# Performance work log

Hardware: AMD Instinct MI355X
Metric: run time of the kernel (lower is better)

The kernel has to match this reference:

```python
import jax, jax.numpy as jnp
import numpy as np

NUM_EXPERTS = 8
EXPERTS_PER_TOK = 2

def setup_inputs() -> dict:
    key = jax.random.key(0)
    k1, k2, k3, k4, k5 = jax.random.split(key, 5)
    B, T, D, F, E = 4, 1024, 2048, 1024, NUM_EXPERTS
    return {
        "x": jax.random.normal(k1, (B, T, D), dtype=jnp.float32),
        "router_w": jax.random.normal(k2, (D, E), dtype=jnp.float32) * 0.02,
        "gate_proj": jax.random.normal(k3, (E, D, F), dtype=jnp.float32) * 0.02,
        "up_proj": jax.random.normal(k4, (E, D, F), dtype=jnp.float32) * 0.02,
        "down_proj": jax.random.normal(k5, (E, F, D), dtype=jnp.float32) * 0.02,
    }

def reference(x, router_w, gate_proj, up_proj, down_proj):
    E, K = NUM_EXPERTS, EXPERTS_PER_TOK
    # Router: softmax over experts, take top-k, renormalize.
    scores = jnp.einsum('btd,de->bte', x, router_w).astype(jnp.float32)
    routing_weights, routing_idx = jax.lax.top_k(jax.nn.softmax(scores, axis=-1), K)
    routing_weights = (routing_weights / jnp.sum(routing_weights, axis=-1, keepdims=True)).astype(x.dtype)
    # one_hot: [B,T,K,E]. Sum over K gives 0/1 dispatch mask [B,T,E]
    # (top-k indices are distinct). Weighted sum gives combine weights.
    onehot = jax.nn.one_hot(routing_idx, E, dtype=x.dtype)
    dispatch_mask = jnp.sum(onehot, axis=2)                      # [B,T,E]
    combine_weights = jnp.einsum('btke,btk->bte', onehot, routing_weights)
    # Dense masked dispatch (same math as original einsum with size-1 I axis).
    dispatched = x[:, :, None, :] * dispatch_mask[..., None]     # [B,T,E,D]
    # SwiGLU FFN for every expert, batched over E.
    gate = jnp.einsum('bted,edf->btef', dispatched, gate_proj)
    up = jnp.einsum('bted,edf->btef', dispatched, up_proj)
    act = jax.nn.silu(gate) * up                                 # [B,T,E,F]
    expert_out = jnp.einsum('btef,efd->bted', act, down_proj)    # [B,T,E,D]
    # Combine: weights already include the dispatch mask via one-hot.
    return jnp.einsum('bted,bte->btd', expert_out, combine_weights)
```

## Files before the change

### kernel.cpp

```cpp
#include <hip/hip_runtime.h>
#include <stdint.h>

#define BT 4096
#define DMODEL 2048
#define FDIM 1024
#define NEXP 8
#define NA (BT * 2)
#define MAXTILES 72
#define NB1 (FDIM / 128)
#define NB2 (DMODEL / 128)
#define GRID1 (MAXTILES * NB1)
#define GRID2 (MAXTILES * NB2)

typedef __attribute__((ext_vector_type(8))) __bf16 bf16x8;
typedef __attribute__((ext_vector_type(4))) float f32x4;

__device__ __forceinline__ unsigned short f2bf(float f) {
  union { float f; unsigned int u; } v; v.f = f;
  unsigned int u = v.u;
  unsigned int r = (u + 0x7fffu + ((u >> 16) & 1u)) >> 16;
  return (unsigned short)r;
}
__device__ __forceinline__ float bf2f(unsigned short h) {
  union { unsigned int u; float f; } v; v.u = ((unsigned int)h) << 16;
  return v.f;
}

__device__ __forceinline__ void g2l16(const void* g, void* l) {
  __builtin_amdgcn_global_load_lds((const __attribute__((address_space(1))) void*)g,
                                   (__attribute__((address_space(3))) void*)l, 16, 0, 0);
}


__global__ void k_router(const float* __restrict__ x, const float* __restrict__ rw,
                         unsigned short* __restrict__ xbf,
                         int* __restrict__ tok_e, float* __restrict__ tok_w) {
  int wid = threadIdx.x >> 6;
  int lane = threadIdx.x & 63;
  int t = blockIdx.x * 4 + wid;
  float acc[8];
#pragma unroll
  for (int e = 0; e < 8; e++) acc[e] = 0.0f;
  const float* xr = x + (size_t)t * DMODEL;
  unsigned short* xbr = xbf + (size_t)t * DMODEL;
#pragma unroll
  for (int d0 = lane * 4; d0 < DMODEL; d0 += 256) {
    float4 xv = *(const float4*)(xr + d0);
    ushort4 o = make_ushort4(f2bf(xv.x), f2bf(xv.y), f2bf(xv.z), f2bf(xv.w));
    *(ushort4*)(xbr + d0) = o;
    const float* xs = &xv.x;
#pragma unroll
    for (int j = 0; j < 4; j++) {
      const float4* r4 = (const float4*)(rw + (size_t)(d0 + j) * NEXP);
      float4 ra = r4[0], rb = r4[1];
      float xj = xs[j];
      acc[0] += xj * ra.x; acc[1] += xj * ra.y; acc[2] += xj * ra.z; acc[3] += xj * ra.w;
      acc[4] += xj * rb.x; acc[5] += xj * rb.y; acc[6] += xj * rb.z; acc[7] += xj * rb.w;
    }
  }
#pragma unroll
  for (int e = 0; e < 8; e++) {
    float v = acc[e];
#pragma unroll
    for (int off = 32; off > 0; off >>= 1) v += __shfl_xor(v, off);
    acc[e] = v;
  }
  if (lane == 0) {
    int e0 = 0; float s0 = acc[0];
#pragma unroll
    for (int e = 1; e < 8; e++) if (acc[e] > s0) { s0 = acc[e]; e0 = e; }
    int e1 = (e0 == 0) ? 1 : 0; float s1 = acc[e1];
#pragma unroll
    for (int e = 0; e < 8; e++) if (e != e0 && acc[e] > s1) { s1 = acc[e]; e1 = e; }
    float w0 = 1.0f / (1.0f + __expf(s1 - s0));
    tok_e[t * 2] = e0; tok_e[t * 2 + 1] = e1;
    tok_w[t * 2] = w0; tok_w[t * 2 + 1] = 1.0f - w0;
  }
}

__global__ void k_scanbuild(const int* __restrict__ tok_e, int* __restrict__ offsets,
                            int* __restrict__ tile_e, int* __restrict__ tile_y,
                            int* __restrict__ ntiles, int* __restrict__ cursors) {
  __shared__ int hist[NEXP];
  int tid = threadIdx.x;
  if (tid < NEXP) hist[tid] = 0;
  __syncthreads();
  for (int i = tid; i < NA; i += 256) atomicAdd(&hist[tok_e[i]], 1);
  __syncthreads();
  if (tid == 0) {
    int s = 0;
    for (int e = 0; e < NEXP; e++) { offsets[e] = s; s += hist[e]; }
    offsets[NEXP] = s;
    int idx = 0;
    for (int e = 0; e < NEXP; e++) {
      int nt = (hist[e] + 127) >> 7;
      for (int y = 0; y < nt; y++) { tile_e[idx] = e; tile_y[idx] = y; idx++; }
    }
    *ntiles = idx;
    for (int i = idx; i < MAXTILES; i++) { tile_e[i] = 0; tile_y[i] = 0; }
  }
  if (tid < NEXP) cursors[tid] = 0;
}

__global__ void k_scatter(const int* __restrict__ tok_e, const float* __restrict__ tok_w,
                          const int* __restrict__ offsets, int* __restrict__ cursors,
                          int* __restrict__ assign_token, float* __restrict__ assign_w,
                          int* __restrict__ tok2pos) {
  int i = blockIdx.x * 256 + threadIdx.x;
  if (i >= NA) return;
  int e = tok_e[i];
  int pos = offsets[e] + atomicAdd(&cursors[e], 1);
  assign_token[pos] = i >> 1;
  assign_w[pos] = tok_w[i];
  tok2pos[i] = pos;
}

__global__ void k_transpose_all(const float* __restrict__ gw, const float* __restrict__ uw,
                                const float* __restrict__ dw,
                                unsigned short* __restrict__ wtg, unsigned short* __restrict__ wtu,
                                unsigned short* __restrict__ wtd) {
  __shared__ float tile[64][65];
  int z = blockIdx.y;
  const float* src; unsigned short* dst; int N;
  if (z < 8)       { src = gw + (size_t)z * DMODEL * FDIM;        dst = wtg + (size_t)z * DMODEL * FDIM;        N = FDIM; }
  else if (z < 16) { src = uw + (size_t)(z - 8) * DMODEL * FDIM;  dst = wtu + (size_t)(z - 8) * DMODEL * FDIM;  N = FDIM; }
  else             { src = dw + (size_t)(z - 16) * FDIM * DMODEL; dst = wtd + (size_t)(z - 16) * FDIM * DMODEL; N = DMODEL; }
  int ntx = N >> 6;
  int bx = blockIdx.x;
  int n0 = (bx % ntx) * 64, k0 = (bx / ntx) * 64;
  int rr = threadIdx.x >> 4, cc = threadIdx.x & 15;
#pragma unroll
  for (int i = 0; i < 4; i++) {
    int k = rr + i * 16;
    float4 v = *(const float4*)(src + (size_t)(k0 + k) * N + n0 + cc * 4);
    tile[k][cc * 4 + 0] = v.x; tile[k][cc * 4 + 1] = v.y;
    tile[k][cc * 4 + 2] = v.z; tile[k][cc * 4 + 3] = v.w;
  }
  __syncthreads();
  int K = (z < 16) ? DMODEL : FDIM;
#pragma unroll
  for (int i = 0; i < 4; i++) {
    int n = rr + i * 16;
    ushort4 o = make_ushort4(f2bf(tile[cc * 4 + 0][n]), f2bf(tile[cc * 4 + 1][n]),
                             f2bf(tile[cc * 4 + 2][n]), f2bf(tile[cc * 4 + 3][n]));
    *(ushort4*)(dst + (size_t)(n0 + n) * K + k0 + cc * 4) = o;
  }
}


__global__ __launch_bounds__(256, 2) void k_gemm1(
    const unsigned short* __restrict__ xbf,
    const unsigned short* __restrict__ wtg,
    const unsigned short* __restrict__ wtu,
    const int* __restrict__ offsets,
    const int* __restrict__ tile_e, const int* __restrict__ tile_y,
    const int* __restrict__ ntiles,
    const int* __restrict__ assign_token,
    unsigned short* __restrict__ act) {
  const int flat = blockIdx.x;
  const int wgid = (flat & 7) * (GRID1 / 8) + (flat >> 3);
  const int ti = wgid % MAXTILES;
  const int nb = wgid / MAXTILES;
  if (ti >= *ntiles) return;
  const int e = tile_e[ti];
  const int row_beg = offsets[e], row_end = offsets[e + 1];
  const int m_base = row_beg + tile_y[ti] * 128;
  const int n_base = nb * 128;

  __shared__ unsigned short As[128][64];
  __shared__ unsigned short Bg[128][64];
  __shared__ unsigned short Bu[128][64];

  const int tid = threadIdx.x;
  const int lane = tid & 63, wid = tid >> 6;
  const int wr = wid >> 1, wc = wid & 1;
  const int srow = wid * 8 + (lane >> 3);
  const int scol_d = (lane & 7) * 8;
  const int scol_s = ((lane & 7) ^ (lane >> 3)) * 8;
  const int sw = (lane & 7) * 8;

  const unsigned short* wg_e = wtg + (size_t)e * FDIM * DMODEL;
  const unsigned short* wu_e = wtu + (size_t)e * FDIM * DMODEL;

  size_t arow[4];
#pragma unroll
  for (int i = 0; i < 4; i++) {
    int slot = m_base + i * 32 + srow;
    if (slot >= row_end) slot = row_end - 1;
    arow[i] = (size_t)assign_token[slot] * DMODEL;
  }

  f32x4 accg[4][4], accu[4][4];
#pragma unroll
  for (int m = 0; m < 4; m++)
#pragma unroll
    for (int n = 0; n < 4; n++) {
      accg[m][n] = f32x4{0.f, 0.f, 0.f, 0.f};
      accu[m][n] = f32x4{0.f, 0.f, 0.f, 0.f};
    }

  for (int k0 = 0; k0 < DMODEL; k0 += 64) {
    __syncthreads();
#pragma unroll
    for (int i = 0; i < 4; i++)
      g2l16(xbf + arow[i] + k0 + scol_s, &As[i * 32 + srow][scol_d]);
#pragma unroll
    for (int i = 0; i < 4; i++)
      g2l16(wg_e + (size_t)(n_base + i * 32 + srow) * DMODEL + k0 + scol_s, &Bg[i * 32 + srow][scol_d]);
#pragma unroll
    for (int i = 0; i < 4; i++)
      g2l16(wu_e + (size_t)(n_base + i * 32 + srow) * DMODEL + k0 + scol_s, &Bu[i * 32 + srow][scol_d]);
    __syncthreads();

#pragma unroll
    for (int kk = 0; kk < 2; kk++) {
      const int ko = kk * 32 + (lane >> 4) * 8;
      bf16x8 a[4], bg[4], bu[4];
#pragma unroll
      for (int m = 0; m < 4; m++)
        a[m] = *(const bf16x8*)&As[wr * 64 + m * 16 + (lane & 15)][ko ^ sw];
#pragma unroll
      for (int n = 0; n < 4; n++) {
        bg[n] = *(const bf16x8*)&Bg[wc * 64 + n * 16 + (lane & 15)][ko ^ sw];
        bu[n] = *(const bf16x8*)&Bu[wc * 64 + n * 16 + (lane & 15)][ko ^ sw];
      }
#pragma unroll
      for (int m = 0; m < 4; m++)
#pragma unroll
        for (int n = 0; n < 4; n++) {
          accg[m][n] = __builtin_amdgcn_mfma_f32_16x16x32_bf16(a[m], bg[n], accg[m][n], 0, 0, 0);
          accu[m][n] = __builtin_amdgcn_mfma_f32_16x16x32_bf16(a[m], bu[n], accu[m][n], 0, 0, 0);
        }
    }
  }

  const int cr = (lane >> 4) * 4;
  const int ccc = lane & 15;
#pragma unroll
  for (int m = 0; m < 4; m++) {
#pragma unroll
    for (int j = 0; j < 4; j++) {
      int slot = m_base + wr * 64 + m * 16 + cr + j;
      if (slot < row_end) {
        unsigned short* dst = act + (size_t)slot * FDIM + n_base + wc * 64 + ccc;
#pragma unroll
        for (int n = 0; n < 4; n++) {
          float g = accg[m][n][j], u = accu[m][n][j];
          float h = (g / (1.0f + __expf(-g))) * u;
          dst[n * 16] = f2bf(h);
        }
      }
    }
  }
}


__global__ __launch_bounds__(256, 2) void k_gemm2(
    const unsigned short* __restrict__ act,
    const unsigned short* __restrict__ wtd,
    const int* __restrict__ offsets,
    const int* __restrict__ tile_e, const int* __restrict__ tile_y,
    const int* __restrict__ ntiles,
    const float* __restrict__ assign_w,
    unsigned short* __restrict__ out_pa) {
  const int flat = blockIdx.x;
  const int wgid = (flat & 7) * (GRID2 / 8) + (flat >> 3);
  const int ti = wgid % MAXTILES;
  const int nb = wgid / MAXTILES;
  if (ti >= *ntiles) return;
  const int e = tile_e[ti];
  const int row_beg = offsets[e], row_end = offsets[e + 1];
  const int m_base = row_beg + tile_y[ti] * 128;
  const int n_base = nb * 128;

  __shared__ unsigned short As[128][64];
  __shared__ unsigned short Bs[128][64];

  const int tid = threadIdx.x;
  const int lane = tid & 63, wid = tid >> 6;
  const int wr = wid >> 1, wc = wid & 1;
  const int srow = wid * 8 + (lane >> 3);
  const int scol_d = (lane & 7) * 8;
  const int scol_s = ((lane & 7) ^ (lane >> 3)) * 8;
  const int sw = (lane & 7) * 8;

  const unsigned short* wd_e = wtd + (size_t)e * DMODEL * FDIM;

  size_t arow[4];
#pragma unroll
  for (int i = 0; i < 4; i++) {
    int slot = m_base + i * 32 + srow;
    if (slot >= row_end) slot = row_end - 1;
    arow[i] = (size_t)slot * FDIM;
  }

  f32x4 acc[4][4];
#pragma unroll
  for (int m = 0; m < 4; m++)
#pragma unroll
    for (int n = 0; n < 4; n++) acc[m][n] = f32x4{0.f, 0.f, 0.f, 0.f};

  for (int k0 = 0; k0 < FDIM; k0 += 64) {
    __syncthreads();
#pragma unroll
    for (int i = 0; i < 4; i++)
      g2l16(act + arow[i] + k0 + scol_s, &As[i * 32 + srow][scol_d]);
#pragma unroll
    for (int i = 0; i < 4; i++)
      g2l16(wd_e + (size_t)(n_base + i * 32 + srow) * FDIM + k0 + scol_s, &Bs[i * 32 + srow][scol_d]);
    __syncthreads();

#pragma unroll
    for (int kk = 0; kk < 2; kk++) {
      const int ko = kk * 32 + (lane >> 4) * 8;
      bf16x8 a[4], b[4];
#pragma unroll
      for (int m = 0; m < 4; m++)
        a[m] = *(const bf16x8*)&As[wr * 64 + m * 16 + (lane & 15)][ko ^ sw];
#pragma unroll
      for (int n = 0; n < 4; n++)
        b[n] = *(const bf16x8*)&Bs[wc * 64 + n * 16 + (lane & 15)][ko ^ sw];
#pragma unroll
      for (int m = 0; m < 4; m++)
#pragma unroll
        for (int n = 0; n < 4; n++)
          acc[m][n] = __builtin_amdgcn_mfma_f32_16x16x32_bf16(a[m], b[n], acc[m][n], 0, 0, 0);
    }
  }

  const int cr = (lane >> 4) * 4;
  const int ccc = lane & 15;
#pragma unroll
  for (int m = 0; m < 4; m++) {
#pragma unroll
    for (int j = 0; j < 4; j++) {
      int slot = m_base + wr * 64 + m * 16 + cr + j;
      if (slot < row_end) {
        float w = assign_w[slot];
        unsigned short* dst = out_pa + (size_t)slot * DMODEL + n_base + wc * 64 + ccc;
#pragma unroll
        for (int n = 0; n < 4; n++)
          dst[n * 16] = f2bf(acc[m][n][j] * w);
      }
    }
  }
}

__global__ void k_combine(const unsigned short* __restrict__ out_pa,
                          const int* __restrict__ tok2pos,
                          float* __restrict__ out) {
  int t = blockIdx.x;
  int p0 = tok2pos[t * 2], p1 = tok2pos[t * 2 + 1];
  int c = threadIdx.x;
  const ushort4* a = (const ushort4*)(out_pa + (size_t)p0 * DMODEL + c * 8);
  const ushort4* b = (const ushort4*)(out_pa + (size_t)p1 * DMODEL + c * 8);
  ushort4 a0 = a[0], a1 = a[1], b0 = b[0], b1 = b[1];
  float* o = out + (size_t)t * DMODEL + c * 8;
  o[0] = bf2f(a0.x) + bf2f(b0.x);
  o[1] = bf2f(a0.y) + bf2f(b0.y);
  o[2] = bf2f(a0.z) + bf2f(b0.z);
  o[3] = bf2f(a0.w) + bf2f(b0.w);
  o[4] = bf2f(a1.x) + bf2f(b1.x);
  o[5] = bf2f(a1.y) + bf2f(b1.y);
  o[6] = bf2f(a1.z) + bf2f(b1.z);
  o[7] = bf2f(a1.w) + bf2f(b1.w);
}


extern "C" void kernel_launch(void* const* d_in, const int* in_sizes, int n_in,
                              void* d_out, int out_size, void* d_ws, size_t ws_size,
                              hipStream_t stream) {
  const float* x  = (const float*)d_in[0];
  const float* rw = (const float*)d_in[1];
  const float* gw = (const float*)d_in[2];
  const float* uw = (const float*)d_in[3];
  const float* dw = (const float*)d_in[4];
  float* out = (float*)d_out;

  char* ws = (char*)d_ws;
  size_t off = 0;
  auto alloc = [&](size_t bytes) {
    size_t o = off;
    off += (bytes + 255) & ~(size_t)255;
    return o;
  };
  unsigned short* xbf    = (unsigned short*)(ws + alloc((size_t)BT * DMODEL * 2));
  unsigned short* wtg    = (unsigned short*)(ws + alloc((size_t)NEXP * FDIM * DMODEL * 2));
  unsigned short* wtu    = (unsigned short*)(ws + alloc((size_t)NEXP * FDIM * DMODEL * 2));
  unsigned short* wtd    = (unsigned short*)(ws + alloc((size_t)NEXP * DMODEL * FDIM * 2));
  unsigned short* act    = (unsigned short*)(ws + alloc((size_t)NA * FDIM * 2));
  unsigned short* out_pa = (unsigned short*)(ws + alloc((size_t)NA * DMODEL * 2));
  int*   offsets = (int*)(ws + alloc((NEXP + 1) * 4));
  int*   cursors = (int*)(ws + alloc(NEXP * 4));
  int*   tok_e   = (int*)(ws + alloc(NA * 4));
  float* tok_w   = (float*)(ws + alloc(NA * 4));
  int*   assign_token = (int*)(ws + alloc(NA * 4));
  float* assign_w     = (float*)(ws + alloc(NA * 4));
  int*   tok2pos      = (int*)(ws + alloc(NA * 4));
  int*   tile_e       = (int*)(ws + alloc(MAXTILES * 4));
  int*   tile_y       = (int*)(ws + alloc(MAXTILES * 4));
  int*   ntiles       = (int*)(ws + alloc(4));
  if (off > ws_size) return;

  k_router<<<BT / 4, 256, 0, stream>>>(x, rw, xbf, tok_e, tok_w);
  k_scanbuild<<<1, 256, 0, stream>>>(tok_e, offsets, tile_e, tile_y, ntiles, cursors);
  k_scatter<<<NA / 256, 256, 0, stream>>>(tok_e, tok_w, offsets, cursors,
                                          assign_token, assign_w, tok2pos);
  k_transpose_all<<<dim3(512, 24), 256, 0, stream>>>(gw, uw, dw, wtg, wtu, wtd);
  k_gemm1<<<GRID1, 256, 0, stream>>>(xbf, wtg, wtu, offsets,
                                     tile_e, tile_y, ntiles, assign_token, act);
  k_gemm2<<<GRID2, 256, 0, stream>>>(act, wtd, offsets,
                                     tile_e, tile_y, ntiles, assign_w, out_pa);
  k_combine<<<BT, 256, 0, stream>>>(out_pa, tok2pos, out);
}
```

Baseline: 320.5 us.

## Double-buffer grouped GEMMs with 256-row tiles and 512-thread blocks

New measurement: 344.9 us. 7.6% more time.

```diff
diff --git a/kernel.cpp b/kernel.cpp
--- a/kernel.cpp
+++ b/kernel.cpp
@@ -6,14 +6,20 @@
 #define FDIM 1024
 #define NEXP 8
 #define NA (BT * 2)
-#define MAXTILES 72
+#define MAXT 40
 #define NB1 (FDIM / 128)
-#define NB2 (DMODEL / 128)
-#define GRID1 (MAXTILES * NB1)
-#define GRID2 (MAXTILES * NB2)
+#define NB2 (DMODEL / 256)
+#define GRID1 (MAXT * NB1)
+#define GRID2 (MAXT * NB2)
+#define NT1 (DMODEL / 64)
+#define NT2 (FDIM / 64)
 
 typedef __attribute__((ext_vector_type(8))) __bf16 bf16x8;
 typedef __attribute__((ext_vector_type(4))) float f32x4;
+
+#define FENCE() asm volatile("" ::: "memory")
+#define BARRIER() do { FENCE(); __builtin_amdgcn_s_barrier(); FENCE(); } while (0)
+#define WAITVM0() asm volatile("s_waitcnt vmcnt(0)" ::: "memory")
 
 __device__ __forceinline__ unsigned short f2bf(float f) {
   union { float f; unsigned int u; } v; v.f = f;
@@ -93,11 +99,11 @@
     offsets[NEXP] = s;
     int idx = 0;
     for (int e = 0; e < NEXP; e++) {
-      int nt = (hist[e] + 127) >> 7;
+      int nt = (hist[e] + 255) >> 8;
       for (int y = 0; y < nt; y++) { tile_e[idx] = e; tile_y[idx] = y; idx++; }
     }
     *ntiles = idx;
-    for (int i = idx; i < MAXTILES; i++) { tile_e[i] = 0; tile_y[i] = 0; }
+    for (int i = idx; i < MAXT; i++) { tile_e[i] = 0; tile_y[i] = 0; }
   }
   if (tid < NEXP) cursors[tid] = 0;
 }
@@ -148,7 +154,7 @@
 }
 
 
-__global__ __launch_bounds__(256, 2) void k_gemm1(
+__global__ __launch_bounds__(512, 2) void k_gemm1(
     const unsigned short* __restrict__ xbf,
     const unsigned short* __restrict__ wtg,
     const unsigned short* __restrict__ wtu,
@@ -159,92 +165,114 @@
     unsigned short* __restrict__ act) {
   const int flat = blockIdx.x;
   const int wgid = (flat & 7) * (GRID1 / 8) + (flat >> 3);
-  const int ti = wgid % MAXTILES;
-  const int nb = wgid / MAXTILES;
+  const int ti = wgid % MAXT;
+  const int nb = wgid / MAXT;
   if (ti >= *ntiles) return;
   const int e = tile_e[ti];
   const int row_beg = offsets[e], row_end = offsets[e + 1];
-  const int m_base = row_beg + tile_y[ti] * 128;
+  const int m_base = row_beg + tile_y[ti] * 256;
   const int n_base = nb * 128;
 
-  __shared__ unsigned short As[128][64];
-  __shared__ unsigned short Bg[128][64];
-  __shared__ unsigned short Bu[128][64];
+  __shared__ unsigned short As[2][256][64];
+  __shared__ unsigned short Bg[2][128][64];
+  __shared__ unsigned short Bu[2][128][64];
 
   const int tid = threadIdx.x;
   const int lane = tid & 63, wid = tid >> 6;
-  const int wr = wid >> 1, wc = wid & 1;
-  const int srow = wid * 8 + (lane >> 3);
-  const int scol_d = (lane & 7) * 8;
-  const int scol_s = ((lane & 7) ^ (lane >> 3)) * 8;
+  const int wm = wid >> 2, wn = wid & 3;
+  const int l15 = lane & 15;
+  const int srow = tid >> 3;
+  const int scol_d = (tid & 7) * 8;
+  const int scol_s = ((tid & 7) ^ (srow & 7)) * 8;
   const int sw = (lane & 7) * 8;
 
-  const unsigned short* wg_e = wtg + (size_t)e * FDIM * DMODEL;
-  const unsigned short* wu_e = wtu + (size_t)e * FDIM * DMODEL;
+  const unsigned short* wg_e = wtg + (size_t)e * FDIM * DMODEL + (size_t)n_base * DMODEL;
+  const unsigned short* wu_e = wtu + (size_t)e * FDIM * DMODEL + (size_t)n_base * DMODEL;
 
   size_t arow[4];
 #pragma unroll
   for (int i = 0; i < 4; i++) {
-    int slot = m_base + i * 32 + srow;
+    int slot = m_base + i * 64 + srow;
     if (slot >= row_end) slot = row_end - 1;
     arow[i] = (size_t)assign_token[slot] * DMODEL;
   }
 
-  f32x4 accg[4][4], accu[4][4];
-#pragma unroll
-  for (int m = 0; m < 4; m++)
-#pragma unroll
-    for (int n = 0; n < 4; n++) {
+  f32x4 accg[8][2], accu[8][2];
+#pragma unroll
+  for (int m = 0; m < 8; m++)
+#pragma unroll
+    for (int n = 0; n < 2; n++) {
       accg[m][n] = f32x4{0.f, 0.f, 0.f, 0.f};
       accu[m][n] = f32x4{0.f, 0.f, 0.f, 0.f};
     }
 
-  for (int k0 = 0; k0 < DMODEL; k0 += 64) {
-    __syncthreads();
+  auto stageA = [&](int buf, int k0) {
 #pragma unroll
     for (int i = 0; i < 4; i++)
-      g2l16(xbf + arow[i] + k0 + scol_s, &As[i * 32 + srow][scol_d]);
-#pragma unroll
-    for (int i = 0; i < 4; i++)
-      g2l16(wg_e + (size_t)(n_base + i * 32 + srow) * DMODEL + k0 + scol_s, &Bg[i * 32 + srow][scol_d]);
-#pragma unroll
-    for (int i = 0; i < 4; i++)
-      g2l16(wu_e + (size_t)(n_base + i * 32 + srow) * DMODEL + k0 + scol_s, &Bu[i * 32 + srow][scol_d]);
-    __syncthreads();
+      g2l16(xbf + arow[i] + k0 + scol_s, &As[buf][i * 64 + srow][scol_d]);
+  };
+  auto stageB = [&](int buf, int k0) {
+#pragma unroll
+    for (int i = 0; i < 2; i++)
+      g2l16(wg_e + (size_t)(i * 64 + srow) * DMODEL + k0 + scol_s, &Bg[buf][i * 64 + srow][scol_d]);
+#pragma unroll
+    for (int i = 0; i < 2; i++)
+      g2l16(wu_e + (size_t)(i * 64 + srow) * DMODEL + k0 + scol_s, &Bu[buf][i * 64 + srow][scol_d]);
+  };
+
+  stageA(0, 0); stageB(0, 0);
+  WAITVM0(); BARRIER();
+
+  for (int t = 0; t < NT1; ++t) {
+    const int cur = t & 1, nxt = cur ^ 1;
+    const int k1 = (t + 1) * 64;
+    const bool pref = (t + 1 < NT1);
 
 #pragma unroll
     for (int kk = 0; kk < 2; kk++) {
       const int ko = kk * 32 + (lane >> 4) * 8;
-      bf16x8 a[4], bg[4], bu[4];
-#pragma unroll
-      for (int m = 0; m < 4; m++)
-        a[m] = *(const bf16x8*)&As[wr * 64 + m * 16 + (lane & 15)][ko ^ sw];
-#pragma unroll
-      for (int n = 0; n < 4; n++) {
-        bg[n] = *(const bf16x8*)&Bg[wc * 64 + n * 16 + (lane & 15)][ko ^ sw];
-        bu[n] = *(const bf16x8*)&Bu[wc * 64 + n * 16 + (lane & 15)][ko ^ sw];
-      }
-#pragma unroll
-      for (int m = 0; m < 4; m++)
-#pragma unroll
-        for (int n = 0; n < 4; n++) {
-          accg[m][n] = __builtin_amdgcn_mfma_f32_16x16x32_bf16(a[m], bg[n], accg[m][n], 0, 0, 0);
-          accu[m][n] = __builtin_amdgcn_mfma_f32_16x16x32_bf16(a[m], bu[n], accu[m][n], 0, 0, 0);
-        }
+      bf16x8 a[8];
+#pragma unroll
+      for (int m = 0; m < 8; m++)
+        a[m] = *(const bf16x8*)&As[cur][wm * 128 + m * 16 + l15][ko ^ sw];
+      bf16x8 b0 = *(const bf16x8*)&Bg[cur][wn * 32 + l15][ko ^ sw];
+      bf16x8 b1 = *(const bf16x8*)&Bg[cur][wn * 32 + 16 + l15][ko ^ sw];
+      if (pref && kk == 0) stageA(nxt, k1);
+      BARRIER();
+      __builtin_amdgcn_s_setprio(1);
+#pragma unroll
+      for (int m = 0; m < 8; m++) {
+        accg[m][0] = __builtin_amdgcn_mfma_f32_16x16x32_bf16(a[m], b0, accg[m][0], 0, 0, 0);
+        accg[m][1] = __builtin_amdgcn_mfma_f32_16x16x32_bf16(a[m], b1, accg[m][1], 0, 0, 0);
+      }
+      __builtin_amdgcn_s_setprio(0);
+      BARRIER();
+      b0 = *(const bf16x8*)&Bu[cur][wn * 32 + l15][ko ^ sw];
+      b1 = *(const bf16x8*)&Bu[cur][wn * 32 + 16 + l15][ko ^ sw];
+      if (pref && kk == 0) stageB(nxt, k1);
+      BARRIER();
+      __builtin_amdgcn_s_setprio(1);
+#pragma unroll
+      for (int m = 0; m < 8; m++) {
+        accu[m][0] = __builtin_amdgcn_mfma_f32_16x16x32_bf16(a[m], b0, accu[m][0], 0, 0, 0);
+        accu[m][1] = __builtin_amdgcn_mfma_f32_16x16x32_bf16(a[m], b1, accu[m][1], 0, 0, 0);
+      }
+      __builtin_amdgcn_s_setprio(0);
+      if (kk == 1 && pref) WAITVM0();
+      BARRIER();
     }
   }
 
   const int cr = (lane >> 4) * 4;
-  const int ccc = lane & 15;
-#pragma unroll
-  for (int m = 0; m < 4; m++) {
+#pragma unroll
+  for (int m = 0; m < 8; m++) {
 #pragma unroll
     for (int j = 0; j < 4; j++) {
-      int slot = m_base + wr * 64 + m * 16 + cr + j;
+      int slot = m_base + wm * 128 + m * 16 + cr + j;
       if (slot < row_end) {
-        unsigned short* dst = act + (size_t)slot * FDIM + n_base + wc * 64 + ccc;
-#pragma unroll
-        for (int n = 0; n < 4; n++) {
+        unsigned short* dst = act + (size_t)slot * FDIM + n_base + wn * 32 + l15;
+#pragma unroll
+        for (int n = 0; n < 2; n++) {
           float g = accg[m][n][j], u = accu[m][n][j];
           float h = (g / (1.0f + __expf(-g))) * u;
           dst[n * 16] = f2bf(h);
@@ -255,7 +283,7 @@
 }
 
 
-__global__ __launch_bounds__(256, 2) void k_gemm2(
+__global__ __launch_bounds__(512, 2) void k_gemm2(
     const unsigned short* __restrict__ act,
     const unsigned short* __restrict__ wtd,
     const int* __restrict__ offsets,
@@ -265,79 +293,105 @@
     unsigned short* __restrict__ out_pa) {
   const int flat = blockIdx.x;
   const int wgid = (flat & 7) * (GRID2 / 8) + (flat >> 3);
-  const int ti = wgid % MAXTILES;
-  const int nb = wgid / MAXTILES;
+  const int ti = wgid % MAXT;
+  const int nb = wgid / MAXT;
   if (ti >= *ntiles) return;
   const int e = tile_e[ti];
   const int row_beg = offsets[e], row_end = offsets[e + 1];
-  const int m_base = row_beg + tile_y[ti] * 128;
-  const int n_base = nb * 128;
-
-  __shared__ unsigned short As[128][64];
-  __shared__ unsigned short Bs[128][64];
+  const int m_base = row_beg + tile_y[ti] * 256;
+  const int n_base = nb * 256;
+
+  __shared__ unsigned short As[2][256][64];
+  __shared__ unsigned short Bs[2][256][64];
 
   const int tid = threadIdx.x;
   const int lane = tid & 63, wid = tid >> 6;
-  const int wr = wid >> 1, wc = wid & 1;
-  const int srow = wid * 8 + (lane >> 3);
-  const int scol_d = (lane & 7) * 8;
-  const int scol_s = ((lane & 7) ^ (lane >> 3)) * 8;
+  const int wm = wid >> 2, wn = wid & 3;
+  const int l15 = lane & 15;
+  const int srow = tid >> 3;
+  const int scol_d = (tid & 7) * 8;
+  const int scol_s = ((tid & 7) ^ (srow & 7)) * 8;
   const int sw = (lane & 7) * 8;
 
-  const unsigned short* wd_e = wtd + (size_t)e * DMODEL * FDIM;
+  const unsigned short* wd_e = wtd + (size_t)e * DMODEL * FDIM + (size_t)n_base * FDIM;
 
   size_t arow[4];
 #pragma unroll
   for (int i = 0; i < 4; i++) {
-    int slot = m_base + i * 32 + srow;
+    int slot = m_base + i * 64 + srow;
     if (slot >= row_end) slot = row_end - 1;
     arow[i] = (size_t)slot * FDIM;
   }
 
-  f32x4 acc[4][4];
-#pragma unroll
-  for (int m = 0; m < 4; m++)
+  f32x4 acc[8][4];
+#pragma unroll
+  for (int m = 0; m < 8; m++)
 #pragma unroll
     for (int n = 0; n < 4; n++) acc[m][n] = f32x4{0.f, 0.f, 0.f, 0.f};
 
-  for (int k0 = 0; k0 < FDIM; k0 += 64) {
-    __syncthreads();
+  auto stageA = [&](int buf, int k0) {
 #pragma unroll
     for (int i = 0; i < 4; i++)
-      g2l16(act + arow[i] + k0 + scol_s, &As[i * 32 + srow][scol_d]);
+      g2l16(act + arow[i] + k0 + scol_s, &As[buf][i * 64 + srow][scol_d]);
+  };
+  auto stageB = [&](int buf, int k0) {
 #pragma unroll
     for (int i = 0; i < 4; i++)
-      g2l16(wd_e + (size_t)(n_base + i * 32 + srow) * FDIM + k0 + scol_s, &Bs[i * 32 + srow][scol_d]);
-    __syncthreads();
+      g2l16(wd_e + (size_t)(i * 64 + srow) * FDIM + k0 + scol_s, &Bs[buf][i * 64 + srow][scol_d]);
+  };
+
+  stageA(0, 0); stageB(0, 0);
+  WAITVM0(); BARRIER();
+
+  for (int t = 0; t < NT2; ++t) {
+    const int cur = t & 1, nxt = cur ^ 1;
+    const int k1 = (t + 1) * 64;
+    const bool pref = (t + 1 < NT2);
 
 #pragma unroll
     for (int kk = 0; kk < 2; kk++) {
       const int ko = kk * 32 + (lane >> 4) * 8;
-      bf16x8 a[4], b[4];
-#pragma unroll
-      for (int m = 0; m < 4; m++)
-        a[m] = *(const bf16x8*)&As[wr * 64 + m * 16 + (lane & 15)][ko ^ sw];
-#pragma unroll
-      for (int n = 0; n < 4; n++)
-        b[n] = *(const bf16x8*)&Bs[wc * 64 + n * 16 + (lane & 15)][ko ^ sw];
-#pragma unroll
-      for (int m = 0; m < 4; m++)
-#pragma unroll
-        for (int n = 0; n < 4; n++)
-          acc[m][n] = __builtin_amdgcn_mfma_f32_16x16x32_bf16(a[m], b[n], acc[m][n], 0, 0, 0);
+      bf16x8 a[8];
+#pragma unroll
+      for (int m = 0; m < 8; m++)
+        a[m] = *(const bf16x8*)&As[cur][wm * 128 + m * 16 + l15][ko ^ sw];
+      bf16x8 b0 = *(const bf16x8*)&Bs[cur][wn * 64 + l15][ko ^ sw];
+      bf16x8 b1 = *(const bf16x8*)&Bs[cur][wn * 64 + 16 + l15][ko ^ sw];
+      if (pref && kk == 0) stageA(nxt, k1);
+      BARRIER();
+      __builtin_amdgcn_s_setprio(1);
+#pragma unroll
+      for (int m = 0; m < 8; m++) {
+        acc[m][0] = __builtin_amdgcn_mfma_f32_16x16x32_bf16(a[m], b0, acc[m][0], 0, 0, 0);
+        acc[m][1] = __builtin_amdgcn_mfma_f32_16x16x32_bf16(a[m], b1, acc[m][1], 0, 0, 0);
+      }
+      __builtin_amdgcn_s_setprio(0);
+      BARRIER();
+      b0 = *(const bf16x8*)&Bs[cur][wn * 64 + 32 + l15][ko ^ sw];
+      b1 = *(const bf16x8*)&Bs[cur][wn * 64 + 48 + l15][ko ^ sw];
+      if (pref && kk == 0) stageB(nxt, k1);
+      BARRIER();
+      __builtin_amdgcn_s_setprio(1);
+#pragma unroll
+      for (int m = 0; m < 8; m++) {
+        acc[m][2] = __builtin_amdgcn_mfma_f32_16x16x32_bf16(a[m], b0, acc[m][2], 0, 0, 0);
+        acc[m][3] = __builtin_amdgcn_mfma_f32_16x16x32_bf16(a[m], b1, acc[m][3], 0, 0, 0);
+      }
+      __builtin_amdgcn_s_setprio(0);
+      if (kk == 1 && pref) WAITVM0();
+      BARRIER();
     }
   }
 
   const int cr = (lane >> 4) * 4;
-  const int ccc = lane & 15;
-#pragma unroll
-  for (int m = 0; m < 4; m++) {
+#pragma unroll
+  for (int m = 0; m < 8; m++) {
 #pragma unroll
     for (int j = 0; j < 4; j++) {
-      int slot = m_base + wr * 64 + m * 16 + cr + j;
+      int slot = m_base + wm * 128 + m * 16 + cr + j;
       if (slot < row_end) {
         float w = assign_w[slot];
-        unsigned short* dst = out_pa + (size_t)slot * DMODEL + n_base + wc * 64 + ccc;
+        unsigned short* dst = out_pa + (size_t)slot * DMODEL + n_base + wn * 64 + l15;
 #pragma unroll
         for (int n = 0; n < 4; n++)
           dst[n * 16] = f2bf(acc[m][n][j] * w);
@@ -397,8 +451,8 @@
   int*   assign_token = (int*)(ws + alloc(NA * 4));
   float* assign_w     = (float*)(ws + alloc(NA * 4));
   int*   tok2pos      = (int*)(ws + alloc(NA * 4));
-  int*   tile_e       = (int*)(ws + alloc(MAXTILES * 4));
-  int*   tile_y       = (int*)(ws + alloc(MAXTILES * 4));
+  int*   tile_e       = (int*)(ws + alloc(MAXT * 4));
+  int*   tile_y       = (int*)(ws + alloc(MAXT * 4));
   int*   ntiles       = (int*)(ws + alloc(4));
   if (off > ws_size) return;
 
@@ -407,9 +461,9 @@
   k_scatter<<<NA / 256, 256, 0, stream>>>(tok_e, tok_w, offsets, cursors,
                                           assign_token, assign_w, tok2pos);
   k_transpose_all<<<dim3(512, 24), 256, 0, stream>>>(gw, uw, dw, wtg, wtu, wtd);
-  k_gemm1<<<GRID1, 256, 0, stream>>>(xbf, wtg, wtu, offsets,
+  k_gemm1<<<GRID1, 512, 0, stream>>>(xbf, wtg, wtu, offsets,
                                      tile_e, tile_y, ntiles, assign_token, act);
-  k_gemm2<<<GRID2, 256, 0, stream>>>(act, wtd, offsets,
+  k_gemm2<<<GRID2, 512, 0, stream>>>(act, wtd, offsets,
                                      tile_e, tile_y, ntiles, assign_w, out_pa);
   k_combine<<<BT, 256, 0, stream>>>(out_pa, tok2pos, out);
 }
```

## Interleave gate/up weights into one B matrix and raise GEMM occupancy

Applied to the files above, without the earlier changes.

Measured after the change: 301.0 us. 6.1% less time.

```diff
diff --git a/kernel.cpp b/kernel.cpp
--- a/kernel.cpp
+++ b/kernel.cpp
@@ -7,10 +7,6 @@
 #define NEXP 8
 #define NA (BT * 2)
 #define MAXTILES 72
-#define NB1 (FDIM / 128)
-#define NB2 (DMODEL / 128)
-#define GRID1 (MAXTILES * NB1)
-#define GRID2 (MAXTILES * NB2)
 
 typedef __attribute__((ext_vector_type(8))) __bf16 bf16x8;
 typedef __attribute__((ext_vector_type(4))) float f32x4;
@@ -117,14 +113,14 @@
 
 __global__ void k_transpose_all(const float* __restrict__ gw, const float* __restrict__ uw,
                                 const float* __restrict__ dw,
-                                unsigned short* __restrict__ wtg, unsigned short* __restrict__ wtu,
+                                unsigned short* __restrict__ wtgu,
                                 unsigned short* __restrict__ wtd) {
   __shared__ float tile[64][65];
   int z = blockIdx.y;
-  const float* src; unsigned short* dst; int N;
-  if (z < 8)       { src = gw + (size_t)z * DMODEL * FDIM;        dst = wtg + (size_t)z * DMODEL * FDIM;        N = FDIM; }
-  else if (z < 16) { src = uw + (size_t)(z - 8) * DMODEL * FDIM;  dst = wtu + (size_t)(z - 8) * DMODEL * FDIM;  N = FDIM; }
-  else             { src = dw + (size_t)(z - 16) * FDIM * DMODEL; dst = wtd + (size_t)(z - 16) * FDIM * DMODEL; N = DMODEL; }
+  const float* src; unsigned short* dst; int N, K, Kd;
+  if (z < 8)       { src = gw + (size_t)z * DMODEL * FDIM;        dst = wtgu + (size_t)z * 2 * FDIM * DMODEL;        N = FDIM;   K = DMODEL; Kd = DMODEL; }
+  else if (z < 16) { src = uw + (size_t)(z - 8) * DMODEL * FDIM;  dst = wtgu + (size_t)(z - 8) * 2 * FDIM * DMODEL;  N = FDIM;   K = DMODEL; Kd = DMODEL; }
+  else             { src = dw + (size_t)(z - 16) * FDIM * DMODEL; dst = wtd + (size_t)(z - 16) * FDIM * DMODEL;      N = DMODEL; K = FDIM;   Kd = FDIM; }
   int ntx = N >> 6;
   int bx = blockIdx.x;
   int n0 = (bx % ntx) * 64, k0 = (bx / ntx) * 64;
@@ -137,39 +133,38 @@
     tile[k][cc * 4 + 2] = v.z; tile[k][cc * 4 + 3] = v.w;
   }
   __syncthreads();
-  int K = (z < 16) ? DMODEL : FDIM;
 #pragma unroll
   for (int i = 0; i < 4; i++) {
     int n = rr + i * 16;
+    int gr = n0 + n;
+    int orow;
+    if (z < 8)       orow = ((gr & ~31) << 1) + (gr & 31);
+    else if (z < 16) orow = ((gr & ~31) << 1) + 32 + (gr & 31);
+    else             orow = gr;
     ushort4 o = make_ushort4(f2bf(tile[cc * 4 + 0][n]), f2bf(tile[cc * 4 + 1][n]),
                              f2bf(tile[cc * 4 + 2][n]), f2bf(tile[cc * 4 + 3][n]));
-    *(ushort4*)(dst + (size_t)(n0 + n) * K + k0 + cc * 4) = o;
-  }
-}
-
-
-__global__ __launch_bounds__(256, 2) void k_gemm1(
+    *(ushort4*)(dst + (size_t)orow * Kd + k0 + cc * 4) = o;
+  }
+}
+
+
+__global__ __launch_bounds__(256, 4) void k_gemm1(
     const unsigned short* __restrict__ xbf,
-    const unsigned short* __restrict__ wtg,
-    const unsigned short* __restrict__ wtu,
+    const unsigned short* __restrict__ wtgu,
     const int* __restrict__ offsets,
     const int* __restrict__ tile_e, const int* __restrict__ tile_y,
     const int* __restrict__ ntiles,
     const int* __restrict__ assign_token,
     unsigned short* __restrict__ act) {
-  const int flat = blockIdx.x;
-  const int wgid = (flat & 7) * (GRID1 / 8) + (flat >> 3);
-  const int ti = wgid % MAXTILES;
-  const int nb = wgid / MAXTILES;
+  const int ti = blockIdx.y;
   if (ti >= *ntiles) return;
   const int e = tile_e[ti];
   const int row_beg = offsets[e], row_end = offsets[e + 1];
   const int m_base = row_beg + tile_y[ti] * 128;
-  const int n_base = nb * 128;
+  const int n_base = blockIdx.x * 128;
 
   __shared__ unsigned short As[128][64];
-  __shared__ unsigned short Bg[128][64];
-  __shared__ unsigned short Bu[128][64];
+  __shared__ unsigned short Bs[128][64];
 
   const int tid = threadIdx.x;
   const int lane = tid & 63, wid = tid >> 6;
@@ -179,8 +174,7 @@
   const int scol_s = ((lane & 7) ^ (lane >> 3)) * 8;
   const int sw = (lane & 7) * 8;
 
-  const unsigned short* wg_e = wtg + (size_t)e * FDIM * DMODEL;
-  const unsigned short* wu_e = wtu + (size_t)e * FDIM * DMODEL;
+  const unsigned short* wb = wtgu + (size_t)e * 2 * FDIM * DMODEL + (size_t)n_base * DMODEL;
 
   size_t arow[4];
 #pragma unroll
@@ -190,14 +184,11 @@
     arow[i] = (size_t)assign_token[slot] * DMODEL;
   }
 
-  f32x4 accg[4][4], accu[4][4];
+  f32x4 acc[4][4];
 #pragma unroll
   for (int m = 0; m < 4; m++)
 #pragma unroll
-    for (int n = 0; n < 4; n++) {
-      accg[m][n] = f32x4{0.f, 0.f, 0.f, 0.f};
-      accu[m][n] = f32x4{0.f, 0.f, 0.f, 0.f};
-    }
+    for (int n = 0; n < 4; n++) acc[m][n] = f32x4{0.f, 0.f, 0.f, 0.f};
 
   for (int k0 = 0; k0 < DMODEL; k0 += 64) {
     __syncthreads();
@@ -206,31 +197,24 @@
       g2l16(xbf + arow[i] + k0 + scol_s, &As[i * 32 + srow][scol_d]);
 #pragma unroll
     for (int i = 0; i < 4; i++)
-      g2l16(wg_e + (size_t)(n_base + i * 32 + srow) * DMODEL + k0 + scol_s, &Bg[i * 32 + srow][scol_d]);
-#pragma unroll
-    for (int i = 0; i < 4; i++)
-      g2l16(wu_e + (size_t)(n_base + i * 32 + srow) * DMODEL + k0 + scol_s, &Bu[i * 32 + srow][scol_d]);
+      g2l16(wb + (size_t)(i * 32 + srow) * DMODEL + k0 + scol_s, &Bs[i * 32 + srow][scol_d]);
     __syncthreads();
 
 #pragma unroll
     for (int kk = 0; kk < 2; kk++) {
       const int ko = kk * 32 + (lane >> 4) * 8;
-      bf16x8 a[4], bg[4], bu[4];
+      bf16x8 a[4], b[4];
 #pragma unroll
       for (int m = 0; m < 4; m++)
         a[m] = *(const bf16x8*)&As[wr * 64 + m * 16 + (lane & 15)][ko ^ sw];
 #pragma unroll
-      for (int n = 0; n < 4; n++) {
-        bg[n] = *(const bf16x8*)&Bg[wc * 64 + n * 16 + (lane & 15)][ko ^ sw];
-        bu[n] = *(const bf16x8*)&Bu[wc * 64 + n * 16 + (lane & 15)][ko ^ sw];
-      }
+      for (int n = 0; n < 4; n++)
+        b[n] = *(const bf16x8*)&Bs[wc * 64 + n * 16 + (lane & 15)][ko ^ sw];
 #pragma unroll
       for (int m = 0; m < 4; m++)
 #pragma unroll
-        for (int n = 0; n < 4; n++) {
-          accg[m][n] = __builtin_amdgcn_mfma_f32_16x16x32_bf16(a[m], bg[n], accg[m][n], 0, 0, 0);
-          accu[m][n] = __builtin_amdgcn_mfma_f32_16x16x32_bf16(a[m], bu[n], accu[m][n], 0, 0, 0);
-        }
+        for (int n = 0; n < 4; n++)
+          acc[m][n] = __builtin_amdgcn_mfma_f32_16x16x32_bf16(a[m], b[n], acc[m][n], 0, 0, 0);
     }
   }
 
@@ -242,10 +226,10 @@
     for (int j = 0; j < 4; j++) {
       int slot = m_base + wr * 64 + m * 16 + cr + j;
       if (slot < row_end) {
-        unsigned short* dst = act + (size_t)slot * FDIM + n_base + wc * 64 + ccc;
-#pragma unroll
-        for (int n = 0; n < 4; n++) {
-          float g = accg[m][n][j], u = accu[m][n][j];
+        unsigned short* dst = act + (size_t)slot * FDIM + (n_base >> 1) + wc * 32 + ccc;
+#pragma unroll
+        for (int n = 0; n < 2; n++) {
+          float g = acc[m][n][j], u = acc[m][n + 2][j];
           float h = (g / (1.0f + __expf(-g))) * u;
           dst[n * 16] = f2bf(h);
         }
@@ -255,7 +239,7 @@
 }
 
 
-__global__ __launch_bounds__(256, 2) void k_gemm2(
+__global__ __launch_bounds__(256, 4) void k_gemm2(
     const unsigned short* __restrict__ act,
     const unsigned short* __restrict__ wtd,
     const int* __restrict__ offsets,
@@ -263,15 +247,12 @@
     const int* __restrict__ ntiles,
     const float* __restrict__ assign_w,
     unsigned short* __restrict__ out_pa) {
-  const int flat = blockIdx.x;
-  const int wgid = (flat & 7) * (GRID2 / 8) + (flat >> 3);
-  const int ti = wgid % MAXTILES;
-  const int nb = wgid / MAXTILES;
+  const int ti = blockIdx.y;
   if (ti >= *ntiles) return;
   const int e = tile_e[ti];
   const int row_beg = offsets[e], row_end = offsets[e + 1];
   const int m_base = row_beg + tile_y[ti] * 128;
-  const int n_base = nb * 128;
+  const int n_base = blockIdx.x * 128;
 
   __shared__ unsigned short As[128][64];
   __shared__ unsigned short Bs[128][64];
@@ -284,7 +265,7 @@
   const int scol_s = ((lane & 7) ^ (lane >> 3)) * 8;
   const int sw = (lane & 7) * 8;
 
-  const unsigned short* wd_e = wtd + (size_t)e * DMODEL * FDIM;
+  const unsigned short* wd_e = wtd + (size_t)e * DMODEL * FDIM + (size_t)n_base * FDIM;
 
   size_t arow[4];
 #pragma unroll
@@ -307,7 +288,7 @@
       g2l16(act + arow[i] + k0 + scol_s, &As[i * 32 + srow][scol_d]);
 #pragma unroll
     for (int i = 0; i < 4; i++)
-      g2l16(wd_e + (size_t)(n_base + i * 32 + srow) * FDIM + k0 + scol_s, &Bs[i * 32 + srow][scol_d]);
+      g2l16(wd_e + (size_t)(i * 32 + srow) * FDIM + k0 + scol_s, &Bs[i * 32 + srow][scol_d]);
     __syncthreads();
 
 #pragma unroll
@@ -385,8 +366,7 @@
     return o;
   };
   unsigned short* xbf    = (unsigned short*)(ws + alloc((size_t)BT * DMODEL * 2));
-  unsigned short* wtg    = (unsigned short*)(ws + alloc((size_t)NEXP * FDIM * DMODEL * 2));
-  unsigned short* wtu    = (unsigned short*)(ws + alloc((size_t)NEXP * FDIM * DMODEL * 2));
+  unsigned short* wtgu   = (unsigned short*)(ws + alloc((size_t)NEXP * 2 * FDIM * DMODEL * 2));
   unsigned short* wtd    = (unsigned short*)(ws + alloc((size_t)NEXP * DMODEL * FDIM * 2));
   unsigned short* act    = (unsigned short*)(ws + alloc((size_t)NA * FDIM * 2));
   unsigned short* out_pa = (unsigned short*)(ws + alloc((size_t)NA * DMODEL * 2));
@@ -406,10 +386,12 @@
   k_scanbuild<<<1, 256, 0, stream>>>(tok_e, offsets, tile_e, tile_y, ntiles, cursors);
   k_scatter<<<NA / 256, 256, 0, stream>>>(tok_e, tok_w, offsets, cursors,
                                           assign_token, assign_w, tok2pos);
-  k_transpose_all<<<dim3(512, 24), 256, 0, stream>>>(gw, uw, dw, wtg, wtu, wtd);
-  k_gemm1<<<GRID1, 256, 0, stream>>>(xbf, wtg, wtu, offsets,
-                                     tile_e, tile_y, ntiles, assign_token, act);
-  k_gemm2<<<GRID2, 256, 0, stream>>>(act, wtd, offsets,
-                                     tile_e, tile_y, ntiles, assign_w, out_pa);
+  k_transpose_all<<<dim3(512, 24), 256, 0, stream>>>(gw, uw, dw, wtgu, wtd);
+  k_gemm1<<<dim3(DMODEL * 2 / 128 / 2, MAXTILES), 256, 0, stream>>>(xbf, wtgu, offsets,
+                                                                    tile_e, tile_y, ntiles,
+                                                                    assign_token, act);
+  k_gemm2<<<dim3(DMODEL / 128, MAXTILES), 256, 0, stream>>>(act, wtd, offsets,
+                                                            tile_e, tile_y, ntiles,
+                                                            assign_w, out_pa);
   k_combine<<<BT, 256, 0, stream>>>(out_pa, tok2pos, out);
 }
```
